# Kernel tuning notes

Measured on AMD Instinct MI355X. Metric: run time of the kernel, lower is better.

## Reference

```python
import jax, jax.numpy as jnp
import numpy as np

POOL = 7
H, W, C = 200, 200, 512
NUM_ROIS = 128


def setup_inputs() -> dict:
    key = jax.random.key(0)
    k1, k2, k3 = jax.random.split(key, 3)
    img = jax.random.normal(k1, (1, H, W, C), dtype=jnp.float32)
    # (x, y, w, h) in feature-map pixels; w,h >= POOL+1 so every bin is >=1px,
    # and x+w <= W, y+h <= H so crops stay in bounds (as the original assumes).
    wh = jax.random.uniform(k2, (1, NUM_ROIS, 2), minval=float(POOL + 1), maxval=64.0)
    xy = jax.random.uniform(k3, (1, NUM_ROIS, 2)) * (jnp.array([W, H], jnp.float32) - wh)
    rois = jnp.concatenate([xy, wh], axis=-1).astype(jnp.float32)
    return {"img": img, "rois": rois, "pool_size": POOL}


def _roi_pool(x, rois, P):
    # x: (H, W, C) feature map; rois: (R, 4) as (x, y, w, h) floats.
    h_dim, w_dim, _ = x.shape
    ks = jnp.arange(P + 1, dtype=jnp.float32)
    rows = jnp.arange(h_dim)
    cols = jnp.arange(w_dim)

    def pool_one(roi):
        rx, ry, rw, rh = roi[0], roi[1], roi[2], roi[3]
        # Bin boundaries: original computes x1 = int(x + ix*w/P), x2 = int(x + (ix+1)*w/P),
        # i.e. contiguous non-overlapping segments [b[k], b[k+1]).
        bx = (rx + ks * (rw / P)).astype(jnp.int32)
        by = (ry + ks * (rh / P)).astype(jnp.int32)
        # Map each row/col to its bin id; out-of-roi pixels -> dummy segment P.
        rid = jnp.searchsorted(by, rows, side='right') - 1
        rid = jnp.where((rid < 0) | (rid >= P), P, rid)
        cid = jnp.searchsorted(bx, cols, side='right') - 1
        cid = jnp.where((cid < 0) | (cid >= P), P, cid)
        # Max-reduce rows into y-bins, then cols into x-bins (separable rect max).
        rm = jax.ops.segment_max(x, rid, num_segments=P + 1)                     # (P+1, W, C) [jy, w, c]
        cm = jax.ops.segment_max(rm.transpose(1, 0, 2), cid, num_segments=P + 1)  # (P+1, P+1, C) [ix, jy, c]
        return cm[:P, :P].transpose(1, 0, 2)  # (jy, ix, c)

    return jax.vmap(pool_one)(rois)  # (R, P, P, C)


def reference(img, rois, pool_size):
    # Output: (1, num_rois, pool_size, pool_size, channels), tf dim ordering.
    out = _roi_pool(img[0], rois[0], pool_size)
    return out[None]
```

## Files before the change

kernel.cpp:

```cpp
#include <hip/hip_runtime.h>


#define IMG_H 200
#define IMG_W 200
#define IMG_C 512
#define POOL 7
#define NROI 128

__global__ __launch_bounds__(128) void roi_pool_kernel(
    const float* __restrict__ img,
    const float* __restrict__ rois,
    float* __restrict__ out)
{
    const int bin = blockIdx.x % (POOL * POOL);
    const int roi = blockIdx.x / (POOL * POOL);
    const int jy = bin / POOL;
    const int ix = bin % POOL;

    const float rx = rois[roi * 4 + 0];
    const float ry = rois[roi * 4 + 1];
    const float rw = rois[roi * 4 + 2];
    const float rh = rois[roi * 4 + 3];

    const float sx = __fdiv_rn(rw, 7.0f);
    const float sy = __fdiv_rn(rh, 7.0f);
    const int x1 = (int)__fadd_rn(rx, __fmul_rn((float)ix,       sx));
    const int x2 = (int)__fadd_rn(rx, __fmul_rn((float)(ix + 1), sx));
    const int y1 = (int)__fadd_rn(ry, __fmul_rn((float)jy,       sy));
    const int y2 = (int)__fadd_rn(ry, __fmul_rn((float)(jy + 1), sy));

    const int c4 = threadIdx.x;
    const float4* __restrict__ img4 = (const float4*)img;

    float4 m = make_float4(-INFINITY, -INFINITY, -INFINITY, -INFINITY);
    for (int y = y1; y < y2; ++y) {
        const float4* __restrict__ row = img4 + ((size_t)y * IMG_W) * (IMG_C / 4) + c4;
        for (int x = x1; x < x2; ++x) {
            float4 v = row[(size_t)x * (IMG_C / 4)];
            m.x = fmaxf(m.x, v.x);
            m.y = fmaxf(m.y, v.y);
            m.z = fmaxf(m.z, v.z);
            m.w = fmaxf(m.w, v.w);
        }
    }

    float4* __restrict__ out4 = (float4*)out;
    out4[((size_t)(roi * POOL + jy) * POOL + ix) * (IMG_C / 4) + c4] = m;
}

extern "C" void kernel_launch(void* const* d_in, const int* in_sizes, int n_in,
                              void* d_out, int out_size, void* d_ws, size_t ws_size,
                              hipStream_t stream) {
    (void)in_sizes; (void)n_in; (void)d_ws; (void)ws_size; (void)out_size;
    const float* img  = (const float*)d_in[0];
    const float* rois = (const float*)d_in[1];
    float* out = (float*)d_out;

    dim3 grid(NROI * POOL * POOL);
    dim3 block(128);
    roi_pool_kernel<<<grid, block, 0, stream>>>(img, rois, out);
}
```

Before: 152.7 us.

## Restructure ROI pooling as image-tile scatter with LDS staging and atomic max

Replaces the per-bin gather kernel with four kernels. The first initialises the output to an encoded minus infinity, the second precomputes bin boundaries, the third scatters, and the fourth decodes. The scatter kernel loads each image tile and channel slice into LDS once with global_load_lds. It then tests every ROI against the tile and reduces the overlapping bins, combining partial maxima across tiles through order-preserving uint atomicMax. This reads each image element once instead of once per overlapping ROI bin, but it adds extra launches, an output init and decode pass, atomics, and a serial scan over all 128 ROIs in every block.

```diff
diff --git a/kernel.cpp b/kernel.cpp
--- a/kernel.cpp
+++ b/kernel.cpp
@@ -1,4 +1,5 @@
 #include <hip/hip_runtime.h>
+#include <stdint.h>
 
 
 #define IMG_H 200
@@ -7,56 +8,169 @@
 #define POOL 7
 #define NROI 128
 
-__global__ __launch_bounds__(128) void roi_pool_kernel(
-    const float* __restrict__ img,
-    const float* __restrict__ rois,
-    float* __restrict__ out)
-{
-    const int bin = blockIdx.x % (POOL * POOL);
-    const int roi = blockIdx.x / (POOL * POOL);
-    const int jy = bin / POOL;
-    const int ix = bin % POOL;
+#define YT 8
+#define XT 16
+#define NYT (IMG_H / YT)
+#define NXT ((IMG_W + XT - 1) / XT)
+#define NQ  (IMG_C / 64)
 
-    const float rx = rois[roi * 4 + 0];
-    const float ry = rois[roi * 4 + 1];
-    const float rw = rois[roi * 4 + 2];
-    const float rh = rois[roi * 4 + 3];
+#define OUT_N (NROI * POOL * POOL * IMG_C)
 
+#define AS1(p) ((const __attribute__((address_space(1))) void*)(p))
+#define AS3(p) ((__attribute__((address_space(3))) void*)(p))
+
+__device__ __forceinline__ float4 max4(float4 a, float4 b) {
+    return make_float4(fmaxf(a.x, b.x), fmaxf(a.y, b.y),
+                       fmaxf(a.z, b.z), fmaxf(a.w, b.w));
+}
+
+__device__ __forceinline__ unsigned enc(float f) {
+    unsigned u = __float_as_uint(f);
+    return ((int)u < 0) ? ~u : (u | 0x80000000u);
+}
+
+__global__ __launch_bounds__(256) void init_kernel(uint4* __restrict__ out) {
+    const unsigned i = blockIdx.x * 256 + threadIdx.x;
+    out[i] = make_uint4(0x007FFFFFu, 0x007FFFFFu, 0x007FFFFFu, 0x007FFFFFu);
+}
+
+__global__ __launch_bounds__(128) void bounds_kernel(
+    const float* __restrict__ rois, int* __restrict__ bnd) {
+    const int r = threadIdx.x;
+    const float rx = rois[r * 4 + 0];
+    const float ry = rois[r * 4 + 1];
+    const float rw = rois[r * 4 + 2];
+    const float rh = rois[r * 4 + 3];
     const float sx = __fdiv_rn(rw, 7.0f);
     const float sy = __fdiv_rn(rh, 7.0f);
-    const int x1 = (int)__fadd_rn(rx, __fmul_rn((float)ix,       sx));
-    const int x2 = (int)__fadd_rn(rx, __fmul_rn((float)(ix + 1), sx));
-    const int y1 = (int)__fadd_rn(ry, __fmul_rn((float)jy,       sy));
-    const int y2 = (int)__fadd_rn(ry, __fmul_rn((float)(jy + 1), sy));
+    #pragma unroll
+    for (int k = 0; k <= 7; ++k) {
+        bnd[r * 16 + k]     = (int)__fadd_rn(rx, __fmul_rn((float)k, sx));
+        bnd[r * 16 + 8 + k] = (int)__fadd_rn(ry, __fmul_rn((float)k, sy));
+    }
+}
 
-    const int c4 = threadIdx.x;
-    const float4* __restrict__ img4 = (const float4*)img;
+__global__ __launch_bounds__(64) void scatter_kernel(
+    const float* __restrict__ img,
+    const int* __restrict__ bnd,
+    unsigned* __restrict__ out)
+{
+    __shared__ float lds[YT * XT * 64];
 
-    float4 m = make_float4(-INFINITY, -INFINITY, -INFINITY, -INFINITY);
-    for (int y = y1; y < y2; ++y) {
-        const float4* __restrict__ row = img4 + ((size_t)y * IMG_W) * (IMG_C / 4) + c4;
-        for (int x = x1; x < x2; ++x) {
-            float4 v = row[(size_t)x * (IMG_C / 4)];
-            m.x = fmaxf(m.x, v.x);
-            m.y = fmaxf(m.y, v.y);
-            m.z = fmaxf(m.z, v.z);
-            m.w = fmaxf(m.w, v.w);
+    const int b  = blockIdx.x;
+    const int q  = b & 7;
+    const int t  = b >> 3;
+    const int ty0 = (t / NXT) * YT;
+    const int tx0 = (t % NXT) * XT;
+    const int ty1 = ty0 + YT;
+    const int tx1 = min(tx0 + XT, IMG_W);
+
+    const int lane = threadIdx.x;
+    const int slot = lane & 15;
+    const int pgrp = lane >> 4;
+
+    const char* gb = (const char*)img + q * 256 + slot * 16;
+    #pragma unroll
+    for (int r = 0; r < YT; ++r) {
+        const size_t rowoff = (size_t)(ty0 + r) * IMG_W;
+        #pragma unroll
+        for (int k = 0; k < 4; ++k) {
+            const int pxg = min(tx0 + 4 * k + pgrp, IMG_W - 1);
+            const char* gp = gb + (rowoff + pxg) * (size_t)2048;
+            __builtin_amdgcn_global_load_lds(AS1(gp),
+                AS3(&lds[(r * XT + 4 * k) * 64]), 16, 0, 0);
         }
     }
 
-    float4* __restrict__ out4 = (float4*)out;
-    out4[((size_t)(roi * POOL + jy) * POOL + ix) * (IMG_C / 4) + c4] = m;
+    unsigned long long m0 = 0ull, m1 = 0ull;
+    for (int roi = 0; roi < NROI; ++roi) {
+        const int bx0 = bnd[roi * 16 + 0];
+        const int bx7 = bnd[roi * 16 + 7];
+        const int by0 = bnd[roi * 16 + 8];
+        const int by7 = bnd[roi * 16 + 15];
+        const bool hit = (bx0 < tx1) & (bx7 > tx0) & (by0 < ty1) & (by7 > ty0);
+        if (roi < 64) m0 |= (unsigned long long)hit << roi;
+        else          m1 |= (unsigned long long)hit << (roi - 64);
+    }
+
+    __builtin_amdgcn_s_waitcnt(0x0F70);
+    if (!(m0 | m1)) return;
+
+    for (int roi = 0; roi < NROI; ++roi) {
+        const bool hit = (roi < 64) ? ((m0 >> roi) & 1ull)
+                                    : ((m1 >> (roi - 64)) & 1ull);
+        if (!hit) continue;
+
+        int bx[8], by[8];
+        #pragma unroll
+        for (int k = 0; k <= 7; ++k) {
+            bx[k] = bnd[roi * 16 + k];
+            by[k] = bnd[roi * 16 + 8 + k];
+        }
+
+        for (int jy = 0; jy < POOL; ++jy) {
+            const int yA = max(by[jy],     ty0);
+            const int yB = min(by[jy + 1], ty1);
+            if (yA >= yB) continue;
+            for (int ix = 0; ix < POOL; ++ix) {
+                const int xA = max(bx[ix],     tx0);
+                const int xB = min(bx[ix + 1], tx1);
+                if (xA >= xB) continue;
+
+                float4 m = make_float4(-INFINITY, -INFINITY, -INFINITY, -INFINITY);
+                const int nIt = (xB - xA + 3) >> 2;
+                for (int yy = yA; yy < yB; ++yy) {
+                    const int rb = (yy - ty0) * XT - tx0;
+                    for (int it = 0; it < nIt; ++it) {
+                        const int px = min(xA + 4 * it + pgrp, xB - 1);
+                        const float4* p = (const float4*)&lds[(rb + px) * 64 + slot * 4];
+                        m = max4(m, *p);
+                    }
+                }
+                m.x = fmaxf(m.x, __shfl_xor(m.x, 16, 64));
+                m.y = fmaxf(m.y, __shfl_xor(m.y, 16, 64));
+                m.z = fmaxf(m.z, __shfl_xor(m.z, 16, 64));
+                m.w = fmaxf(m.w, __shfl_xor(m.w, 16, 64));
+                m.x = fmaxf(m.x, __shfl_xor(m.x, 32, 64));
+                m.y = fmaxf(m.y, __shfl_xor(m.y, 32, 64));
+                m.z = fmaxf(m.z, __shfl_xor(m.z, 32, 64));
+                m.w = fmaxf(m.w, __shfl_xor(m.w, 32, 64));
+
+                if (pgrp == 0) {
+                    unsigned* o = out +
+                        (((unsigned)roi * 49 + jy * 7 + ix) * IMG_C + q * 64 + slot * 4);
+                    atomicMax(o + 0, enc(m.x));
+                    atomicMax(o + 1, enc(m.y));
+                    atomicMax(o + 2, enc(m.z));
+                    atomicMax(o + 3, enc(m.w));
+                }
+            }
+        }
+    }
+}
+
+__global__ __launch_bounds__(256) void decode_kernel(unsigned* __restrict__ out) {
+    const unsigned i = (blockIdx.x * 256 + threadIdx.x) * 4;
+    uint4 u = *(const uint4*)(out + i);
+    float4 f;
+    f.x = (u.x & 0x80000000u) ? __uint_as_float(u.x ^ 0x80000000u) : __uint_as_float(~u.x);
+    f.y = (u.y & 0x80000000u) ? __uint_as_float(u.y ^ 0x80000000u) : __uint_as_float(~u.y);
+    f.z = (u.z & 0x80000000u) ? __uint_as_float(u.z ^ 0x80000000u) : __uint_as_float(~u.z);
+    f.w = (u.w & 0x80000000u) ? __uint_as_float(u.w ^ 0x80000000u) : __uint_as_float(~u.w);
+    *(float4*)(out + i) = f;
 }
 
 extern "C" void kernel_launch(void* const* d_in, const int* in_sizes, int n_in,
                               void* d_out, int out_size, void* d_ws, size_t ws_size,
                               hipStream_t stream) {
-    (void)in_sizes; (void)n_in; (void)d_ws; (void)ws_size; (void)out_size;
+    (void)in_sizes; (void)n_in; (void)ws_size; (void)out_size;
     const float* img  = (const float*)d_in[0];
     const float* rois = (const float*)d_in[1];
-    float* out = (float*)d_out;
+    unsigned* out = (unsigned*)d_out;
+    int* bnd = (int*)d_ws;
 
-    dim3 grid(NROI * POOL * POOL);
-    dim3 block(128);
-    roi_pool_kernel<<<grid, block, 0, stream>>>(img, rois, out);
+    init_kernel<<<dim3(OUT_N / 4 / 256), dim3(256), 0, stream>>>((uint4*)out);
+    bounds_kernel<<<dim3(1), dim3(128), 0, stream>>>(rois, bnd);
+    scatter_kernel<<<dim3(NYT * NXT * NQ), dim3(64), 0, stream>>>(img, bnd, out);
+    decode_kernel<<<dim3(OUT_N / 4 / 256), dim3(256), 0, stream>>>(out);
 }
```

New measurement: 313.4 us. +105.3%, slower.
